# Kernel optimization log

Measured on AMD Instinct MI355X. Metric: run time of the kernel, lower is better.

## Reference

```python
import jax, jax.numpy as jnp
from jax import lax
import numpy as np

INPUT_SIZE = 64
HIDDEN = 256
HORIZON = 24
NUM_CLASSES = 5
B, T = 256, 512


def _lstm_layer(x, W_ih, W_hh, b_ih, b_hh):
    """Single-layer LSTM, PyTorch gate order (i, f, g, o).
    x: [B, T, D_in] -> returns (outputs [B, T, H], final_h [B, H])."""
    Bsz = x.shape[0]
    H = W_hh.shape[1]
    # Precompute all input-side gate projections in one GEMM: [B, T, 4H]
    xg = jnp.einsum('btd,gd->btg', x, W_ih) + (b_ih + b_hh)
    xg = jnp.swapaxes(xg, 0, 1)  # [T, B, 4H] for scan

    h0 = jnp.zeros((Bsz, H), dtype=x.dtype)
    c0 = jnp.zeros((Bsz, H), dtype=x.dtype)

    def step(carry, xg_t):
        h, c = carry
        gates = xg_t + h @ W_hh.T  # [B, 4H]
        i, f, g, o = jnp.split(gates, 4, axis=-1)
        i = jax.nn.sigmoid(i)
        f = jax.nn.sigmoid(f)
        g = jnp.tanh(g)
        o = jax.nn.sigmoid(o)
        c = f * c + i * g
        h = o * jnp.tanh(c)
        return (h, c), h

    (h_n, c_n), hs = lax.scan(step, (h0, c0), xg)
    return jnp.swapaxes(hs, 0, 1), h_n


def setup_inputs() -> dict:
    key = jax.random.key(0)
    ks = jax.random.split(key, 12)
    s_in = 1.0 / np.sqrt(HIDDEN)
    x = jax.random.normal(ks[0], (B, T, INPUT_SIZE), dtype=jnp.float32)
    # layer 0 (input_size -> hidden), layer 1 (hidden -> hidden)
    W_ih0 = jax.random.uniform(ks[1], (4 * HIDDEN, INPUT_SIZE), jnp.float32, -s_in, s_in)
    W_hh0 = jax.random.uniform(ks[2], (4 * HIDDEN, HIDDEN), jnp.float32, -s_in, s_in)
    b_ih0 = jax.random.uniform(ks[3], (4 * HIDDEN,), jnp.float32, -s_in, s_in)
    b_hh0 = jax.random.uniform(ks[4], (4 * HIDDEN,), jnp.float32, -s_in, s_in)
    W_ih1 = jax.random.uniform(ks[5], (4 * HIDDEN, HIDDEN), jnp.float32, -s_in, s_in)
    W_hh1 = jax.random.uniform(ks[6], (4 * HIDDEN, HIDDEN), jnp.float32, -s_in, s_in)
    b_ih1 = jax.random.uniform(ks[7], (4 * HIDDEN,), jnp.float32, -s_in, s_in)
    b_hh1 = jax.random.uniform(ks[8], (4 * HIDDEN,), jnp.float32, -s_in, s_in)
    W_head = jax.random.uniform(ks[9], (HORIZON * NUM_CLASSES, HIDDEN), jnp.float32, -s_in, s_in)
    b_head = jax.random.uniform(ks[10], (HORIZON * NUM_CLASSES,), jnp.float32, -s_in, s_in)
    return {"x": x, "W_ih0": W_ih0, "W_hh0": W_hh0, "b_ih0": b_ih0, "b_hh0": b_hh0,
            "W_ih1": W_ih1, "W_hh1": W_hh1, "b_ih1": b_ih1, "b_hh1": b_hh1,
            "W_head": W_head, "b_head": b_head}


def reference(x, W_ih0, W_hh0, b_ih0, b_hh0, W_ih1, W_hh1, b_ih1, b_hh1, W_head, b_head):
    # 2-layer unidirectional LSTM (eval mode: inter-layer dropout disabled)
    out0, _ = _lstm_layer(x, W_ih0, W_hh0, b_ih0, b_hh0)
    _, h_last = _lstm_layer(out0, W_ih1, W_hh1, b_ih1, b_hh1)  # h_n[-1]: [B, H]
    logits = h_last @ W_head.T + b_head  # [B, horizon*num_classes]
    return logits.reshape(x.shape[0], HORIZON, NUM_CLASSES)
```

## Files before the change

kernel.cpp:

```cpp
#include <hip/hip_runtime.h>

typedef _Float16 half_t;
typedef _Float16 half8 __attribute__((ext_vector_type(8)));
typedef float f32x4 __attribute__((ext_vector_type(4)));
typedef unsigned long long u64;
typedef unsigned int u32;
typedef unsigned short u16;

#define GROUPS 16
#define WPG 8
#define NWG 128
#define THREADS 512
#define TSTEPS 512

#define W0_HALVES (8*8*10*64*8)
#define W1_HALVES (8*8*16*64*8)
#define X_HALVES  (512*16*1024)
#define HX_U32    (2*GROUPS*4096)

__device__ __forceinline__ float sigm(float x){ return 1.f/(1.f+__expf(-x)); }
__device__ __forceinline__ float tanh_fast(float x){ float e=__expf(2.f*x); return 1.f - 2.f/(e+1.f); }

__global__ void prep_w0(const float* __restrict__ Wih, const float* __restrict__ Whh,
                        half_t* __restrict__ dst){
  int idx = blockIdx.x*blockDim.x + threadIdx.x;
  if (idx >= 8*8*10*64) return;
  int lane = idx & 63;
  int kc = (idx >> 6) % 10;
  int jw = idx / 640;
  int tr = lane & 15, kg = lane >> 4;
  int grow = (tr&3)*256 + jw*4 + (tr>>2);
  int k0 = kc*32 + kg*8;
  half_t* d = dst + (size_t)idx*8;
#pragma unroll
  for (int jj=0;jj<8;jj++){
    int k = k0 + jj;
    float v = (k < 64) ? Wih[grow*64 + k] : Whh[grow*256 + (k - 64)];
    d[jj] = (half_t)v;
  }
}

__global__ void prep_w1(const float* __restrict__ Wih, const float* __restrict__ Whh,
                        half_t* __restrict__ dst){
  int idx = blockIdx.x*blockDim.x + threadIdx.x;
  if (idx >= 8*8*16*64) return;
  int lane = idx & 63;
  int kc = (idx >> 6) & 15;
  int jw = idx >> 10;
  int tr = lane & 15, kg = lane >> 4;
  int grow = (tr&3)*256 + jw*4 + (tr>>2);
  int k0 = kc*32 + kg*8;
  half_t* d = dst + (size_t)idx*8;
#pragma unroll
  for (int jj=0;jj<8;jj++){
    int k = k0 + jj;
    float v = (k < 256) ? Wih[grow*256 + k] : Whh[grow*256 + (k - 256)];
    d[jj] = (half_t)v;
  }
}

__global__ void prep_x(const float* __restrict__ x, half_t* __restrict__ xblk){
  int idx = blockIdx.x*blockDim.x + threadIdx.x;
  if (idx >= 512*16*8*16) return;
  int b = idx & 15;
  int k8 = (idx >> 4) & 7;
  int g = (idx >> 7) & 15;
  int t = idx >> 11;
  const float* src = x + ((size_t)(g*16+b)*512 + (size_t)t)*64 + k8*8;
  half_t* d = xblk + (size_t)idx*8;
#pragma unroll
  for (int jj=0;jj<8;jj++) d[jj] = (half_t)src[jj];
}

__device__ __forceinline__ void poll_stage(const u64* s, half_t* sb, int tid, u32 want){
  u64 v[4];
  int ok = 0;
  for (int tries = 0; !ok && tries < (1<<20); ++tries){
    ok = 1;
#pragma unroll
    for (int i = 0; i < 4; ++i)
      v[i] = __hip_atomic_load(s + tid + i*512, __ATOMIC_RELAXED, __HIP_MEMORY_SCOPE_AGENT);
#pragma unroll
    for (int i = 0; i < 4; ++i)
      ok &= (int)((((u32)(v[i] >> 16) & 0xFFFFu) >= want) & (((u32)(v[i] >> 48)) >= want));
  }
#pragma unroll
  for (int i = 0; i < 4; ++i){
    int m = tid + i*512;
    int jw2 = m >> 5, kg2 = (m >> 3) & 3, lc0 = (2*m) & 15;
    int hh2 = jw2*4 + kg2;
    half_t* d = sb + ((hh2 >> 3)*16 + lc0)*8 + (hh2 & 7);
    d[0] = __builtin_bit_cast(half_t, (u16)(v[i] & 0xFFFFu));
    d[8] = __builtin_bit_cast(half_t, (u16)((v[i] >> 32) & 0xFFFFu));
  }
}

__global__ __launch_bounds__(THREADS, 1) void lstm_dist(
    const half_t* __restrict__ W0blk, const half_t* __restrict__ W1blk,
    const half_t* __restrict__ xblk,
    u32* __restrict__ h0x, u32* __restrict__ h1x,
    const float* __restrict__ b_ih0, const float* __restrict__ b_hh0,
    const float* __restrict__ b_ih1, const float* __restrict__ b_hh1,
    const float* __restrict__ W_head, const float* __restrict__ b_head,
    float* __restrict__ out)
{
  __shared__ __align__(16) half_t hbuf[2][8192];

  const int tid = threadIdx.x;
  const int wave = tid >> 6, lane = tid & 63;
  const int lcol = lane & 15, kg = lane >> 4;
  const int bid = blockIdx.x;
  const int g = bid >> 3, j = bid & 7;
  const int jw = j*8 + wave;

  half8 a0[10], a1[16];
#pragma unroll
  for (int kc = 0; kc < 10; ++kc)
    a0[kc] = *(const half8*)(W0blk + ((size_t)(jw*10 + kc)*64 + lane)*8);
#pragma unroll
  for (int kc = 0; kc < 16; ++kc)
    a1[kc] = *(const half8*)(W1blk + ((size_t)(jw*16 + kc)*64 + lane)*8);
#pragma unroll
  for (int kc = 0; kc < 10; ++kc) asm volatile("" : "+v"(a0[kc]));
#pragma unroll
  for (int kc = 0; kc < 16; ++kc) asm volatile("" : "+v"(a1[kc]));

  const int hh = jw*4 + kg;
  const int eoff = jw*64 + lane;
  f32x4 bias0, bias1;
#pragma unroll
  for (int ri = 0; ri < 4; ++ri){
    bias0[ri] = b_ih0[ri*256+hh] + b_hh0[ri*256+hh];
    bias1[ri] = b_ih1[ri*256+hh] + b_hh1[ri*256+hh];
  }

  for (int i = tid; i < 8192; i += THREADS) ((u32*)hbuf)[i] = 0u;

  float c0 = 0.f, c1 = 0.f;
  half8 xf0, xf1;
  {
    const half_t* xs = xblk + (size_t)g*1024;
    xf0 = *(const half8*)(xs + ((0*4+kg)*16 + lcol)*8);
    xf1 = *(const half8*)(xs + ((1*4+kg)*16 + lcol)*8);
  }
  __syncthreads();

  for (int q = 0; q <= TSTEPS; ++q){
    const int sslot = (q+1)&1, dslot = q&1;
    const u32 want = (u32)q;

    if (q > 0)
      poll_stage((const u64*)(h0x + (size_t)(sslot*GROUPS + g)*4096),
                 hbuf[sslot], tid, want);
    __syncthreads();

    const half_t* cb = hbuf[sslot];
    half8 h0f[8];
#pragma unroll
    for (int c = 0; c < 8; ++c)
      h0f[c] = *(const half8*)(cb + ((c*4+kg)*16 + lcol)*8);

    if (q < TSTEPS){
      __builtin_amdgcn_s_setprio(1);
      f32x4 acc = bias0;
      acc = __builtin_amdgcn_mfma_f32_16x16x32_f16(a0[0], xf0, acc, 0,0,0);
      acc = __builtin_amdgcn_mfma_f32_16x16x32_f16(a0[1], xf1, acc, 0,0,0);
#pragma unroll
      for (int c = 0; c < 8; ++c)
        acc = __builtin_amdgcn_mfma_f32_16x16x32_f16(a0[c+2], h0f[c], acc, 0,0,0);
      float ig=sigm(acc[0]), fg=sigm(acc[1]), gg=tanh_fast(acc[2]), og=sigm(acc[3]);
      c0 = fg*c0 + ig*gg;
      float hv = og*tanh_fast(c0);
      u32 sv = ((u32)(q+1) << 16) | (u32)__builtin_bit_cast(u16, (half_t)hv);
      __hip_atomic_store(h0x + (size_t)(dslot*GROUPS + g)*4096 + eoff, sv,
                         __ATOMIC_RELAXED, __HIP_MEMORY_SCOPE_AGENT);
      __builtin_amdgcn_s_setprio(0);
      __builtin_amdgcn_sched_barrier(0);
    }

    if (q > 1)
      poll_stage((const u64*)(h1x + (size_t)(sslot*GROUPS + g)*4096),
                 hbuf[sslot] + 4096, tid, want);
    __syncthreads();

    if (q >= 1){
      __builtin_amdgcn_s_setprio(1);
      f32x4 acc = bias1;
#pragma unroll
      for (int c = 0; c < 8; ++c)
        acc = __builtin_amdgcn_mfma_f32_16x16x32_f16(a1[c], h0f[c], acc, 0,0,0);
#pragma unroll
      for (int c = 0; c < 8; ++c){
        half8 h1f = *(const half8*)(cb + 4096 + ((c*4+kg)*16 + lcol)*8);
        acc = __builtin_amdgcn_mfma_f32_16x16x32_f16(a1[c+8], h1f, acc, 0,0,0);
      }
      float ig=sigm(acc[0]), fg=sigm(acc[1]), gg=tanh_fast(acc[2]), og=sigm(acc[3]);
      c1 = fg*c1 + ig*gg;
      float hv = og*tanh_fast(c1);
      u32 sv = ((u32)(q+1) << 16) | (u32)__builtin_bit_cast(u16, (half_t)hv);
      __hip_atomic_store(h1x + (size_t)(dslot*GROUPS + g)*4096 + eoff, sv,
                         __ATOMIC_RELAXED, __HIP_MEMORY_SCOPE_AGENT);
      __builtin_amdgcn_s_setprio(0);
    }

    if (q+1 < TSTEPS){
      const half_t* xs = xblk + (size_t)((q+1)*16 + g)*1024;
      xf0 = *(const half8*)(xs + ((0*4+kg)*16 + lcol)*8);
      xf1 = *(const half8*)(xs + ((1*4+kg)*16 + lcol)*8);
    }
  }

  __syncthreads();

  {
    poll_stage((const u64*)(h1x + (size_t)(0*GROUPS + g)*4096),
               hbuf[0], tid, (u32)(TSTEPS + 1));
    __syncthreads();

    if (tid < 240){
      int bl = 2*j + (tid >= 120 ? 1 : 0);
      int o = tid % 120;
      float s2 = b_head[o];
      const float* wr = W_head + (size_t)o*256;
#pragma unroll 4
      for (int k8 = 0; k8 < 32; ++k8){
        half8 hv = *(const half8*)(hbuf[0] + (k8*16 + bl)*8);
#pragma unroll
        for (int jj = 0; jj < 8; ++jj)
          s2 += (float)hv[jj] * wr[k8*8 + jj];
      }
      out[((size_t)(g*16 + bl))*120 + o] = s2;
    }
  }
}

extern "C" void kernel_launch(void* const* d_in, const int* in_sizes, int n_in,
                              void* d_out, int out_size, void* d_ws, size_t ws_size,
                              hipStream_t stream){
  const float* x     = (const float*)d_in[0];
  const float* W_ih0 = (const float*)d_in[1];
  const float* W_hh0 = (const float*)d_in[2];
  const float* b_ih0 = (const float*)d_in[3];
  const float* b_hh0 = (const float*)d_in[4];
  const float* W_ih1 = (const float*)d_in[5];
  const float* W_hh1 = (const float*)d_in[6];
  const float* b_ih1 = (const float*)d_in[7];
  const float* b_hh1 = (const float*)d_in[8];
  const float* W_head= (const float*)d_in[9];
  const float* b_head= (const float*)d_in[10];
  float* out = (float*)d_out;

  half_t* W0blk = (half_t*)d_ws;
  half_t* W1blk = W0blk + W0_HALVES;
  half_t* xblk  = W1blk + W1_HALVES;
  u32*    h0x   = (u32*)(xblk + X_HALVES);
  u32*    h1x   = h0x + HX_U32;

  (void)hipMemsetAsync(h0x, 0, (size_t)HX_U32*2*4, stream);

  hipLaunchKernelGGL(prep_w0, dim3(160), dim3(256), 0, stream, W_ih0, W_hh0, W0blk);
  hipLaunchKernelGGL(prep_w1, dim3(256), dim3(256), 0, stream, W_ih1, W_hh1, W1blk);
  hipLaunchKernelGGL(prep_x,  dim3(4096), dim3(256), 0, stream, x, xblk);

  hipLaunchKernelGGL(lstm_dist, dim3(NWG), dim3(THREADS), 0, stream,
                     W0blk, W1blk, xblk, h0x, h1x,
                     b_ih0, b_hh0, b_ih1, b_hh1, W_head, b_head, out);
}
```

Measured before the change: 1.420 ms.

## Process four batch groups per workgroup and merge layer polls per step

The LSTM work split drops from 128 to 32 workgroups. Each workgroup now handles four batch groups (CPS=4) with the same weight slice and per-group cell states and LDS buffers. The two poll/sync phases per timestep are merged into one barrier that polls both layers' hidden states. The goal is to cut the number of communicating workgroups and barriers, in exchange for four times more serial MFMA work per workgroup per step. It also moves to 128KB of dynamic LDS. Merging layer 1's poll with layer 0's removes the overlap between layer-0 compute and waiting on layer 1.

```diff
diff --git a/kernel.cpp b/kernel.cpp
--- a/kernel.cpp
+++ b/kernel.cpp
@@ -9,7 +9,8 @@
 
 #define GROUPS 16
 #define WPG 8
-#define NWG 128
+#define CPS 4
+#define NWG 32
 #define THREADS 512
 #define TSTEPS 512
 
@@ -17,6 +18,8 @@
 #define W1_HALVES (8*8*16*64*8)
 #define X_HALVES  (512*16*1024)
 #define HX_U32    (2*GROUPS*4096)
+
+#define LDS_TOTAL (CPS*2*16384)
 
 __device__ __forceinline__ float sigm(float x){ return 1.f/(1.f+__expf(-x)); }
 __device__ __forceinline__ float tanh_fast(float x){ float e=__expf(2.f*x); return 1.f - 2.f/(e+1.f); }
@@ -104,13 +107,14 @@
     const float* __restrict__ W_head, const float* __restrict__ b_head,
     float* __restrict__ out)
 {
-  __shared__ __align__(16) half_t hbuf[2][8192];
+  extern __shared__ __align__(16) char smem[];
+  half_t* hb = (half_t*)smem;
 
   const int tid = threadIdx.x;
   const int wave = tid >> 6, lane = tid & 63;
   const int lcol = lane & 15, kg = lane >> 4;
   const int bid = blockIdx.x;
-  const int g = bid >> 3, j = bid & 7;
+  const int st = bid >> 3, j = bid & 7;
   const int jw = j*8 + wave;
 
   half8 a0[10], a1[16];
@@ -134,14 +138,18 @@
     bias1[ri] = b_ih1[ri*256+hh] + b_hh1[ri*256+hh];
   }
 
-  for (int i = tid; i < 8192; i += THREADS) ((u32*)hbuf)[i] = 0u;
-
-  float c0 = 0.f, c1 = 0.f;
-  half8 xf0, xf1;
-  {
-    const half_t* xs = xblk + (size_t)g*1024;
-    xf0 = *(const half8*)(xs + ((0*4+kg)*16 + lcol)*8);
-    xf1 = *(const half8*)(xs + ((1*4+kg)*16 + lcol)*8);
+  for (int i = tid; i < LDS_TOTAL/4; i += THREADS) ((u32*)hb)[i] = 0u;
+
+  float c0[CPS], c1[CPS];
+#pragma unroll
+  for (int ch = 0; ch < CPS; ++ch){ c0[ch] = 0.f; c1[ch] = 0.f; }
+
+  half8 xf[CPS][2];
+#pragma unroll
+  for (int ch = 0; ch < CPS; ++ch){
+    const half_t* xs = xblk + (size_t)(st*CPS + ch)*1024;
+    xf[ch][0] = *(const half8*)(xs + ((0*4+kg)*16 + lcol)*8);
+    xf[ch][1] = *(const half8*)(xs + ((1*4+kg)*16 + lcol)*8);
   }
   __syncthreads();
 
@@ -149,87 +157,107 @@
     const int sslot = (q+1)&1, dslot = q&1;
     const u32 want = (u32)q;
 
-    if (q > 0)
-      poll_stage((const u64*)(h0x + (size_t)(sslot*GROUPS + g)*4096),
-                 hbuf[sslot], tid, want);
+    if (q > 0){
+#pragma unroll
+      for (int ch = 0; ch < CPS; ++ch){
+        const int g = st*CPS + ch;
+        half_t* sb = hb + (size_t)(ch*2 + sslot)*8192;
+        poll_stage((const u64*)(h0x + (size_t)(sslot*GROUPS + g)*4096), sb, tid, want);
+        if (q > 1)
+          poll_stage((const u64*)(h1x + (size_t)(sslot*GROUPS + g)*4096), sb + 4096, tid, want);
+      }
+    }
     __syncthreads();
 
-    const half_t* cb = hbuf[sslot];
-    half8 h0f[8];
-#pragma unroll
-    for (int c = 0; c < 8; ++c)
-      h0f[c] = *(const half8*)(cb + ((c*4+kg)*16 + lcol)*8);
-
-    if (q < TSTEPS){
-      __builtin_amdgcn_s_setprio(1);
-      f32x4 acc = bias0;
-      acc = __builtin_amdgcn_mfma_f32_16x16x32_f16(a0[0], xf0, acc, 0,0,0);
-      acc = __builtin_amdgcn_mfma_f32_16x16x32_f16(a0[1], xf1, acc, 0,0,0);
+#pragma unroll
+    for (int ch = 0; ch < CPS; ++ch){
+      const int g = st*CPS + ch;
+      const half_t* cb = hb + (size_t)(ch*2 + sslot)*8192;
+      half8 h0f[8];
 #pragma unroll
       for (int c = 0; c < 8; ++c)
-        acc = __builtin_amdgcn_mfma_f32_16x16x32_f16(a0[c+2], h0f[c], acc, 0,0,0);
-      float ig=sigm(acc[0]), fg=sigm(acc[1]), gg=tanh_fast(acc[2]), og=sigm(acc[3]);
-      c0 = fg*c0 + ig*gg;
-      float hv = og*tanh_fast(c0);
-      u32 sv = ((u32)(q+1) << 16) | (u32)__builtin_bit_cast(u16, (half_t)hv);
-      __hip_atomic_store(h0x + (size_t)(dslot*GROUPS + g)*4096 + eoff, sv,
-                         __ATOMIC_RELAXED, __HIP_MEMORY_SCOPE_AGENT);
-      __builtin_amdgcn_s_setprio(0);
-      __builtin_amdgcn_sched_barrier(0);
-    }
-
-    if (q > 1)
-      poll_stage((const u64*)(h1x + (size_t)(sslot*GROUPS + g)*4096),
-                 hbuf[sslot] + 4096, tid, want);
-    __syncthreads();
-
-    if (q >= 1){
-      __builtin_amdgcn_s_setprio(1);
-      f32x4 acc = bias1;
-#pragma unroll
-      for (int c = 0; c < 8; ++c)
-        acc = __builtin_amdgcn_mfma_f32_16x16x32_f16(a1[c], h0f[c], acc, 0,0,0);
-#pragma unroll
-      for (int c = 0; c < 8; ++c){
-        half8 h1f = *(const half8*)(cb + 4096 + ((c*4+kg)*16 + lcol)*8);
-        acc = __builtin_amdgcn_mfma_f32_16x16x32_f16(a1[c+8], h1f, acc, 0,0,0);
-      }
-      float ig=sigm(acc[0]), fg=sigm(acc[1]), gg=tanh_fast(acc[2]), og=sigm(acc[3]);
-      c1 = fg*c1 + ig*gg;
-      float hv = og*tanh_fast(c1);
-      u32 sv = ((u32)(q+1) << 16) | (u32)__builtin_bit_cast(u16, (half_t)hv);
-      __hip_atomic_store(h1x + (size_t)(dslot*GROUPS + g)*4096 + eoff, sv,
-                         __ATOMIC_RELAXED, __HIP_MEMORY_SCOPE_AGENT);
-      __builtin_amdgcn_s_setprio(0);
+        h0f[c] = *(const half8*)(cb + ((c*4+kg)*16 + lcol)*8);
+
+      if (q < TSTEPS){
+        __builtin_amdgcn_s_setprio(1);
+        f32x4 acc = bias0;
+        acc = __builtin_amdgcn_mfma_f32_16x16x32_f16(a0[0], xf[ch][0], acc, 0,0,0);
+        acc = __builtin_amdgcn_mfma_f32_16x16x32_f16(a0[1], xf[ch][1], acc, 0,0,0);
+#pragma unroll
+        for (int c = 0; c < 8; ++c)
+          acc = __builtin_amdgcn_mfma_f32_16x16x32_f16(a0[c+2], h0f[c], acc, 0,0,0);
+        float ig=sigm(acc[0]), fg=sigm(acc[1]), gg=tanh_fast(acc[2]), og=sigm(acc[3]);
+        c0[ch] = fg*c0[ch] + ig*gg;
+        float hv = og*tanh_fast(c0[ch]);
+        u32 sv = ((u32)(q+1) << 16) | (u32)__builtin_bit_cast(u16, (half_t)hv);
+        __hip_atomic_store(h0x + (size_t)(dslot*GROUPS + g)*4096 + eoff, sv,
+                           __ATOMIC_RELAXED, __HIP_MEMORY_SCOPE_AGENT);
+        __builtin_amdgcn_s_setprio(0);
+        __builtin_amdgcn_sched_barrier(0);
+      }
+
+      if (q >= 1){
+        __builtin_amdgcn_s_setprio(1);
+        f32x4 acc = bias1;
+#pragma unroll
+        for (int c = 0; c < 8; ++c)
+          acc = __builtin_amdgcn_mfma_f32_16x16x32_f16(a1[c], h0f[c], acc, 0,0,0);
+#pragma unroll
+        for (int c = 0; c < 8; ++c){
+          half8 h1f = *(const half8*)(cb + 4096 + ((c*4+kg)*16 + lcol)*8);
+          acc = __builtin_amdgcn_mfma_f32_16x16x32_f16(a1[c+8], h1f, acc, 0,0,0);
+        }
+        float ig=sigm(acc[0]), fg=sigm(acc[1]), gg=tanh_fast(acc[2]), og=sigm(acc[3]);
+        c1[ch] = fg*c1[ch] + ig*gg;
+        float hv = og*tanh_fast(c1[ch]);
+        u32 sv = ((u32)(q+1) << 16) | (u32)__builtin_bit_cast(u16, (half_t)hv);
+        __hip_atomic_store(h1x + (size_t)(dslot*GROUPS + g)*4096 + eoff, sv,
+                           __ATOMIC_RELAXED, __HIP_MEMORY_SCOPE_AGENT);
+        __builtin_amdgcn_s_setprio(0);
+        __builtin_amdgcn_sched_barrier(0);
+      }
     }
 
     if (q+1 < TSTEPS){
-      const half_t* xs = xblk + (size_t)((q+1)*16 + g)*1024;
-      xf0 = *(const half8*)(xs + ((0*4+kg)*16 + lcol)*8);
-      xf1 = *(const half8*)(xs + ((1*4+kg)*16 + lcol)*8);
+#pragma unroll
+      for (int ch = 0; ch < CPS; ++ch){
+        const half_t* xs = xblk + (size_t)((q+1)*16 + st*CPS + ch)*1024;
+        xf[ch][0] = *(const half8*)(xs + ((0*4+kg)*16 + lcol)*8);
+        xf[ch][1] = *(const half8*)(xs + ((1*4+kg)*16 + lcol)*8);
+      }
     }
   }
 
   __syncthreads();
 
   {
-    poll_stage((const u64*)(h1x + (size_t)(0*GROUPS + g)*4096),
-               hbuf[0], tid, (u32)(TSTEPS + 1));
+#pragma unroll
+    for (int ch = 0; ch < CPS; ++ch){
+      const int g = st*CPS + ch;
+      poll_stage((const u64*)(h1x + (size_t)(0*GROUPS + g)*4096),
+                 hb + (size_t)(ch*2)*8192, tid, (u32)(TSTEPS + 1));
+    }
     __syncthreads();
 
     if (tid < 240){
       int bl = 2*j + (tid >= 120 ? 1 : 0);
       int o = tid % 120;
-      float s2 = b_head[o];
       const float* wr = W_head + (size_t)o*256;
+      float bh = b_head[o];
+#pragma unroll
+      for (int ch = 0; ch < CPS; ++ch){
+        const int g = st*CPS + ch;
+        const half_t* hbch = hb + (size_t)(ch*2)*8192;
+        float s2 = bh;
 #pragma unroll 4
-      for (int k8 = 0; k8 < 32; ++k8){
-        half8 hv = *(const half8*)(hbuf[0] + (k8*16 + bl)*8);
-#pragma unroll
-        for (int jj = 0; jj < 8; ++jj)
-          s2 += (float)hv[jj] * wr[k8*8 + jj];
-      }
-      out[((size_t)(g*16 + bl))*120 + o] = s2;
+        for (int k8 = 0; k8 < 32; ++k8){
+          half8 hv = *(const half8*)(hbch + (k8*16 + bl)*8);
+#pragma unroll
+          for (int jj = 0; jj < 8; ++jj)
+            s2 += (float)hv[jj] * wr[k8*8 + jj];
+        }
+        out[((size_t)(g*16 + bl))*120 + o] = s2;
+      }
     }
   }
 }
@@ -262,7 +290,10 @@
   hipLaunchKernelGGL(prep_w1, dim3(256), dim3(256), 0, stream, W_ih1, W_hh1, W1blk);
   hipLaunchKernelGGL(prep_x,  dim3(4096), dim3(256), 0, stream, x, xblk);
 
-  hipLaunchKernelGGL(lstm_dist, dim3(NWG), dim3(THREADS), 0, stream,
+  (void)hipFuncSetAttribute((const void*)lstm_dist,
+                            hipFuncAttributeMaxDynamicSharedMemorySize, LDS_TOTAL);
+
+  hipLaunchKernelGGL(lstm_dist, dim3(NWG), dim3(THREADS), LDS_TOTAL, stream,
                      W0blk, W1blk, xblk, h0x, h1x,
                      b_ih0, b_hh0, b_ih1, b_hh1, W_head, b_head, out);
 }
```

Result: slower. 4.342 ms (+205.7%).
